# Kernel optimization log

Measured on AMD Instinct MI355X. Metric: run time of the kernel, lower is better.

## Reference

```python
import jax, jax.numpy as jnp
import numpy as np

V = 32000      # vocab_size
CTX = 1024     # context_length
D = 768        # n_embd
H = 12         # n_heads
HD = D // H    # head_dim
L = 6          # n_layers
DFF = 4 * D
B, S = 2, 1024
EPS = 1e-5


def _layernorm(x, w, b):
    mu = jnp.mean(x, axis=-1, keepdims=True)
    var = jnp.mean(jnp.square(x - mu), axis=-1, keepdims=True)
    return (x - mu) * jax.lax.rsqrt(var + EPS) * w + b


def setup_inputs() -> dict:
    key = jax.random.key(0)
    ks = iter(jax.random.split(key, 32))
    s = 0.02
    idx = jax.random.randint(next(ks), (B, S), 0, V)
    p = {
        "idx": idx,
        "tok_emb": jax.random.normal(next(ks), (V, D), jnp.float32) * s,
        "pos_emb": jax.random.normal(next(ks), (CTX, D), jnp.float32) * s,
        "ln1_w": jnp.ones((L, D)), "ln1_b": jnp.zeros((L, D)),
        "Wq": jax.random.normal(next(ks), (L, D, D), jnp.float32) * s,
        "bq": jnp.zeros((L, D)),
        "Wk": jax.random.normal(next(ks), (L, D, D), jnp.float32) * s,
        "bk": jnp.zeros((L, D)),
        "Wv": jax.random.normal(next(ks), (L, D, D), jnp.float32) * s,
        "bv": jnp.zeros((L, D)),
        "Wo": jax.random.normal(next(ks), (L, D, D), jnp.float32) * s,
        "bo": jnp.zeros((L, D)),
        "ln2_w": jnp.ones((L, D)), "ln2_b": jnp.zeros((L, D)),
        "W1": jax.random.normal(next(ks), (L, D, DFF), jnp.float32) * s,
        "b1": jnp.zeros((L, DFF)),
        "W2": jax.random.normal(next(ks), (L, DFF, D), jnp.float32) * s,
        "b2": jnp.zeros((L, D)),
        "lnf_w": jnp.ones((D,)), "lnf_b": jnp.zeros((D,)),
        "lm_head_w": jax.random.normal(next(ks), (D, V), jnp.float32) * s,
    }
    return p


def _forward(idx, tok_emb, pos_emb, ln1_w, ln1_b, Wq, bq, Wk, bk, Wv, bv,
             Wo, bo, ln2_w, ln2_b, W1, b1, W2, b2, lnf_w, lnf_b, lm_head_w):
    b, s = idx.shape
    x = tok_emb[idx] + pos_emb[:s]  # [B,S,D]
    mask = jnp.tril(jnp.ones((s, s), dtype=bool))  # causal
    scale = 1.0 / np.sqrt(HD)
    for l in range(L):
        # --- attention ---
        h = _layernorm(x, ln1_w[l], ln1_b[l])
        q = (h @ Wq[l] + bq[l]).reshape(b, s, H, HD).transpose(0, 2, 1, 3)
        k = (h @ Wk[l] + bk[l]).reshape(b, s, H, HD).transpose(0, 2, 1, 3)
        v = (h @ Wv[l] + bv[l]).reshape(b, s, H, HD).transpose(0, 2, 1, 3)
        att = jnp.einsum('bhqd,bhkd->bhqk', q, k) * scale
        att = jnp.where(mask, att, -jnp.inf)
        att = jax.nn.softmax(att, axis=-1)
        y = jnp.einsum('bhqk,bhkd->bhqd', att, v)
        y = y.transpose(0, 2, 1, 3).reshape(b, s, D)
        x = x + y @ Wo[l] + bo[l]
        # --- MLP ---
        h2 = _layernorm(x, ln2_w[l], ln2_b[l])
        x = x + jax.nn.relu(h2 @ W1[l] + b1[l]) @ W2[l] + b2[l]
    logits = _layernorm(x, lnf_w, lnf_b) @ lm_head_w  # [B,S,V]
    return logits


def reference(idx, tok_emb, pos_emb, ln1_w, ln1_b, Wq, bq, Wk, bk, Wv, bv,
              Wo, bo, ln2_w, ln2_b, W1, b1, W2, b2, lnf_w, lnf_b, lm_head_w):
    return _forward(idx, tok_emb, pos_emb, ln1_w, ln1_b, Wq, bq, Wk, bk, Wv,
                    bv, Wo, bo, ln2_w, ln2_b, W1, b1, W2, b2, lnf_w, lnf_b,
                    lm_head_w)
```

## Files before the change

### kernel.cpp

```cpp
#include <hip/hip_runtime.h>
#include <hip/hip_bf16.h>
#include <math.h>

#define D 768
#define NH 12
#define HD 64
#define NL 6
#define DFF 3072
#define BB 2
#define SS 1024
#define NROWS (BB*SS)
#define VOCAB 32000
#define QKVN (3*D)
#define LN_EPS 1e-5f

typedef __attribute__((ext_vector_type(8))) short bf16x8;
typedef __attribute__((ext_vector_type(4))) float f32x4;

typedef __attribute__((address_space(1))) const unsigned char* gas_ptr;
typedef __attribute__((address_space(3))) unsigned char* las_ptr;

__device__ __forceinline__ void load_lds16(const void* g, void* l) {
    __builtin_amdgcn_global_load_lds((gas_ptr)g, (las_ptr)l, 16, 0, 0);
}

__device__ __forceinline__ void storeOut(float* p, float v) { *p = v; }
__device__ __forceinline__ void storeOut(__hip_bfloat16* p, float v) { *p = __float2bfloat16(v); }
__device__ __forceinline__ ushort f2bs(float f) {
    __hip_bfloat16 h = __float2bfloat16(f);
    return *(ushort*)&h;
}

__global__ void embed_kernel(const int* __restrict__ idx, const float* __restrict__ tok,
                             const float* __restrict__ pos, float* __restrict__ x) {
    int row = blockIdx.x;
    int s = row % SS;
    int t = idx[row];
    for (int c = threadIdx.x; c < D; c += blockDim.x)
        x[row*D + c] = tok[(size_t)t*D + c] + pos[s*D + c];
}

template<typename OT>
__global__ __launch_bounds__(256) void layernorm_kernel(const float* __restrict__ x,
                                                        const float* __restrict__ w,
                                                        const float* __restrict__ b,
                                                        OT* __restrict__ out) {
    int row = blockIdx.x;
    __shared__ float l1[4], l2[4];
    int base = row * D;
    float vals[3];
    float s1 = 0.f, s2 = 0.f;
#pragma unroll
    for (int i = 0; i < 3; i++) {
        float v = x[base + threadIdx.x + i*256];
        vals[i] = v; s1 += v; s2 += v*v;
    }
#pragma unroll
    for (int o = 32; o > 0; o >>= 1) {
        s1 += __shfl_down(s1, o, 64);
        s2 += __shfl_down(s2, o, 64);
    }
    if ((threadIdx.x & 63) == 0) { l1[threadIdx.x >> 6] = s1; l2[threadIdx.x >> 6] = s2; }
    __syncthreads();
    float sum   = l1[0] + l1[1] + l1[2] + l1[3];
    float sumsq = l2[0] + l2[1] + l2[2] + l2[3];
    float mu  = sum * (1.f / D);
    float var = sumsq * (1.f / D) - mu * mu;
    float inv = rsqrtf(var + LN_EPS);
#pragma unroll
    for (int i = 0; i < 3; i++) {
        int c = threadIdx.x + i*256;
        storeOut(&out[base + c], (vals[i] - mu) * inv * w[c] + b[c]);
    }
}

__global__ __launch_bounds__(256) void transpose_cvt(const float* __restrict__ src,
                                                     __hip_bfloat16* __restrict__ dst,
                                                     int K, int N,
                                                     size_t srcLayerStride, size_t dstLayerStride,
                                                     int dstRowOff) {
    int l = blockIdx.z;
    src += (size_t)l * srcLayerStride;
    dst += (size_t)l * dstLayerStride + (size_t)dstRowOff * K;
    __shared__ float t[32][33];
    int k0 = blockIdx.x*32, n0 = blockIdx.y*32;
    int tx = threadIdx.x & 31, ty = threadIdx.x >> 5;
    for (int i = ty; i < 32; i += 8) t[i][tx] = src[(size_t)(k0+i)*N + n0+tx];
    __syncthreads();
    for (int i = ty; i < 32; i += 8) dst[(size_t)(n0+i)*K + k0+tx] = __float2bfloat16(t[tx][i]);
}

__global__ __launch_bounds__(256) void vtrans_kernel(const ushort* __restrict__ qkv,
                                                     ushort* __restrict__ vt) {
    int bh = blockIdx.z;
    int st = blockIdx.y;
    int dt = blockIdx.x;
    __shared__ ushort t[32][33];
    int tx = threadIdx.x & 31, ty = threadIdx.x >> 5;
    int b = bh / NH, h = bh % NH;
    int s0 = st*32, d0 = dt*32;
    for (int i = ty; i < 32; i += 8)
        t[i][tx] = qkv[(size_t)(b*SS + s0+i)*QKVN + 2*D + h*HD + d0 + tx];
    __syncthreads();
    for (int i = ty; i < 32; i += 8)
        vt[((size_t)bh*HD + d0+i)*SS + s0 + tx] = t[tx][i];
}

__global__ void pack_qkv_bias(const float* __restrict__ bq, const float* __restrict__ bk,
                              const float* __restrict__ bv, float* __restrict__ dst) {
    int l = blockIdx.y;
    int i = blockIdx.x*256 + threadIdx.x;
    dst[l*QKVN + i]         = bq[l*D + i];
    dst[l*QKVN + D + i]     = bk[l*D + i];
    dst[l*QKVN + 2*D + i]   = bv[l*D + i];
}

#define GSTAGE(buf, k0) do {                                                     \
    _Pragma("unroll")                                                            \
    for (int i_ = 0; i_ < BM/64; i_++) {                                         \
        int rt_ = wid*(BM/4) + i_*16;                                            \
        load_lds16(A + (size_t)(bm + rt_ + lrow)*K + (k0) + lcol,                \
                   &As[buf][rt_][0]);                                            \
    }                                                                            \
    _Pragma("unroll")                                                            \
    for (int i_ = 0; i_ < BN/64; i_++) {                                         \
        int rt_ = wid*(BN/4) + i_*16;                                            \
        load_lds16(BT + (size_t)(bn + rt_ + lrow)*K + (k0) + lcol,               \
                   &Bs[buf][rt_][0]);                                            \
    } } while (0)

template<int BM, int BN, int CMAJ, typename OT, int RELU, int RESID, int HASB>
__global__ __launch_bounds__(256) void gemm_mfma(const ushort* __restrict__ A,
                                                 const ushort* __restrict__ BT,
                                                 const float* __restrict__ bias,
                                                 const float* __restrict__ X,
                                                 OT* __restrict__ C,
                                                 int N, int K, int gx, int gy) {
    constexpr int WTM = BM/2, WTN = BN/2;
    constexpr int FRM = BM/32, FRN = BN/32;
    __shared__ ushort As[2][BM][32];
    __shared__ ushort Bs[2][BN][32];

    int id = blockIdx.x;
    int swz = (id & 7) * (gridDim.x >> 3) + (id >> 3);
    int bx, by;
    if (CMAJ) { bx = swz / gy; by = swz - bx * gy; }
    else      { by = swz / gx; bx = swz - by * gx; }
    int bm = by * BM, bn = bx * BN;

    int tid = threadIdx.x;
    int lane = tid & 63, wid = tid >> 6;
    int wr = wid >> 1, wc = wid & 1;
    int lrow = lane >> 2;
    int lcol = (((lane & 3) ^ (lrow & 3)) * 8);
    int fr = lane & 15, fc = lane >> 4;

    f32x4 acc[FRM][FRN];
#pragma unroll
    for (int i = 0; i < FRM; i++)
#pragma unroll
        for (int j = 0; j < FRN; j++)
#pragma unroll
            for (int r = 0; r < 4; r++) acc[i][j][r] = 0.f;

    GSTAGE(0, 0);
    asm volatile("s_waitcnt vmcnt(0)" ::: "memory");
    __syncthreads();

    int cur = 0;
    for (int t = 0; t < K/32; t++) {
        if (t*32 + 32 < K) GSTAGE(cur^1, t*32 + 32);
        bf16x8 af[FRM], bf[FRN];
#pragma unroll
        for (int mi = 0; mi < FRM; mi++)
            af[mi] = *(const bf16x8*)&As[cur][wr*WTM + mi*16 + fr][(fc ^ (fr & 3))*8];
#pragma unroll
        for (int ni = 0; ni < FRN; ni++)
            bf[ni] = *(const bf16x8*)&Bs[cur][wc*WTN + ni*16 + fr][(fc ^ (fr & 3))*8];
        __builtin_amdgcn_s_setprio(1);
#pragma unroll
        for (int mi = 0; mi < FRM; mi++)
#pragma unroll
            for (int ni = 0; ni < FRN; ni++)
                acc[mi][ni] = __builtin_amdgcn_mfma_f32_16x16x32_bf16(af[mi], bf[ni], acc[mi][ni], 0, 0, 0);
        __builtin_amdgcn_s_setprio(0);
        asm volatile("s_waitcnt vmcnt(0)" ::: "memory");
        __syncthreads();
        cur ^= 1;
    }
#pragma unroll
    for (int mi = 0; mi < FRM; mi++) {
#pragma unroll
        for (int r = 0; r < 4; r++) {
            int row = bm + wr*WTM + mi*16 + fc*4 + r;
#pragma unroll
            for (int ni = 0; ni < FRN; ni++) {
                int col = bn + wc*WTN + ni*16 + fr;
                float v = acc[mi][ni][r];
                if (HASB) v += bias[col];
                if (RESID) v += X[(size_t)row * N + col];
                if (RELU) v = fmaxf(v, 0.f);
                storeOut(&C[(size_t)row * N + col], v);
            }
        }
    }
}

#define KVSTAGE(buf, kv0) do {                                                   \
    _Pragma("unroll")                                                            \
    for (int j_ = 0; j_ < 2; j_++) {                                             \
        int r_ = w*16 + j_*8 + srow8;                                            \
        load_lds16(qkv + (size_t)(b*SS + (kv0) + r_)*QKVN + D + h*HD + schunk*8, \
                   &Ks[buf][w*16 + j_*8][0]);                                    \
        load_lds16(vt + ((size_t)(b*NH + h)*HD + r_)*SS + (kv0) + schunk*8,      \
                   &Vs[buf][w*16 + j_*8][0]);                                    \
    } } while (0)

__global__ __launch_bounds__(256) void attn_mfma(const ushort* __restrict__ qkv,
                                                 const ushort* __restrict__ vt,
                                                 __hip_bfloat16* __restrict__ y) {
    const int bx = blockIdx.x;
    const int qt = 15 - (bx & 15);
    const int h  = (bx >> 4) % NH;
    const int b  = bx / (16*NH);
    const int tid  = threadIdx.x;
    const int lane = tid & 63, w = tid >> 6;
    const int fr = lane & 15, fc = lane >> 4;

    __shared__ ushort Qs[64][64];
    __shared__ ushort Ks[2][64][64];
    __shared__ ushort Vs[2][64][64];
    __shared__ ushort Ps[4][16][72];

    const int q0 = qt * 64;
    const int srow8  = lane >> 3;
    const int schunk = (lane & 7) ^ srow8;

#pragma unroll
    for (int j = 0; j < 2; j++) {
        int r = w*16 + j*8 + srow8;
        load_lds16(qkv + (size_t)(b*SS + q0 + r)*QKVN + h*HD + schunk*8, &Qs[w*16 + j*8][0]);
    }
    KVSTAGE(0, 0);
    asm volatile("s_waitcnt vmcnt(0)" ::: "memory");
    __syncthreads();
    bf16x8 qf[2];
#pragma unroll
    for (int s = 0; s < 2; s++)
        qf[s] = *(const bf16x8*)&Qs[w*16 + fr][((s*4 + fc) ^ (fr & 7))*8];

    f32x4 oacc[4];
#pragma unroll
    for (int ni = 0; ni < 4; ni++)
#pragma unroll
        for (int r = 0; r < 4; r++) oacc[ni][r] = 0.f;
    float m[4] = {-INFINITY, -INFINITY, -INFINITY, -INFINITY};
    float l[4] = {0.f, 0.f, 0.f, 0.f};

    int cur = 0;
    for (int kt = 0; kt <= qt; kt++) {
        if (kt < qt) KVSTAGE(cur^1, (kt+1)*64);
        f32x4 sacc[4];
#pragma unroll
        for (int ni = 0; ni < 4; ni++)
#pragma unroll
            for (int r = 0; r < 4; r++) sacc[ni][r] = 0.f;
#pragma unroll
        for (int ni = 0; ni < 4; ni++)
#pragma unroll
            for (int s = 0; s < 2; s++) {
                bf16x8 kf = *(const bf16x8*)&Ks[cur][ni*16 + fr][((s*4 + fc) ^ (fr & 7))*8];
                sacc[ni] = __builtin_amdgcn_mfma_f32_16x16x32_bf16(qf[s], kf, sacc[ni], 0, 0, 0);
            }
        if (kt == qt) {
#pragma unroll
            for (int ni = 0; ni < 4; ni++)
#pragma unroll
                for (int r = 0; r < 4; r++) {
                    float v = sacc[ni][r] * 0.125f;
                    sacc[ni][r] = (ni*16 + fr > w*16 + fc*4 + r) ? -INFINITY : v;
                }
        } else {
#pragma unroll
            for (int ni = 0; ni < 4; ni++)
#pragma unroll
                for (int r = 0; r < 4; r++) sacc[ni][r] *= 0.125f;
        }
        float p[4][4];
#pragma unroll
        for (int r = 0; r < 4; r++) {
            float mx = fmaxf(fmaxf(sacc[0][r], sacc[1][r]), fmaxf(sacc[2][r], sacc[3][r]));
#pragma unroll
            for (int o = 1; o < 16; o <<= 1) mx = fmaxf(mx, __shfl_xor(mx, o, 64));
            float mn = fmaxf(m[r], mx);
            float fac = __expf(m[r] - mn);
            float rs = 0.f;
#pragma unroll
            for (int ni = 0; ni < 4; ni++) {
                float pv = __expf(sacc[ni][r] - mn);
                p[ni][r] = pv;
                rs += pv;
            }
#pragma unroll
            for (int o = 1; o < 16; o <<= 1) rs += __shfl_xor(rs, o, 64);
            l[r] = l[r] * fac + rs;
            m[r] = mn;
#pragma unroll
            for (int ni = 0; ni < 4; ni++) oacc[ni][r] *= fac;
        }
#pragma unroll
        for (int ni = 0; ni < 4; ni++)
#pragma unroll
            for (int r = 0; r < 4; r++)
                Ps[w][fc*4 + r][ni*16 + fr] = f2bs(p[ni][r]);
        bf16x8 pa[2];
#pragma unroll
        for (int s = 0; s < 2; s++) pa[s] = *(const bf16x8*)&Ps[w][fr][s*32 + fc*8];
#pragma unroll
        for (int ni = 0; ni < 4; ni++)
#pragma unroll
            for (int s = 0; s < 2; s++) {
                bf16x8 vf = *(const bf16x8*)&Vs[cur][ni*16 + fr][((s*4 + fc) ^ (fr & 7))*8];
                oacc[ni] = __builtin_amdgcn_mfma_f32_16x16x32_bf16(pa[s], vf, oacc[ni], 0, 0, 0);
            }
        asm volatile("s_waitcnt vmcnt(0)" ::: "memory");
        __syncthreads();
        cur ^= 1;
    }
#pragma unroll
    for (int r = 0; r < 4; r++) {
        float rinv = 1.f / l[r];
        int row = b*SS + q0 + w*16 + fc*4 + r;
#pragma unroll
        for (int ni = 0; ni < 4; ni++)
            y[(size_t)row*D + h*HD + ni*16 + fr] = __float2bfloat16(oacc[ni][r] * rinv);
    }
}

extern "C" void kernel_launch(void* const* d_in, const int* in_sizes, int n_in,
                              void* d_out, int out_size, void* d_ws, size_t ws_size,
                              hipStream_t stream) {
    const int*   idx  = (const int*)d_in[0];
    const float* tok  = (const float*)d_in[1];
    const float* pos  = (const float*)d_in[2];
    const float* ln1w = (const float*)d_in[3];
    const float* ln1b = (const float*)d_in[4];
    const float* Wq   = (const float*)d_in[5];
    const float* bq   = (const float*)d_in[6];
    const float* Wk   = (const float*)d_in[7];
    const float* bk   = (const float*)d_in[8];
    const float* Wv   = (const float*)d_in[9];
    const float* bv   = (const float*)d_in[10];
    const float* Wo   = (const float*)d_in[11];
    const float* bo   = (const float*)d_in[12];
    const float* ln2w = (const float*)d_in[13];
    const float* ln2b = (const float*)d_in[14];
    const float* W1   = (const float*)d_in[15];
    const float* b1   = (const float*)d_in[16];
    const float* W2   = (const float*)d_in[17];
    const float* b2   = (const float*)d_in[18];
    const float* lnfw = (const float*)d_in[19];
    const float* lnfb = (const float*)d_in[20];
    const float* lmw  = (const float*)d_in[21];
    float* out = (float*)d_out;

    char* p = (char*)d_ws;
    __hip_bfloat16* qkvT = (__hip_bfloat16*)p; p += (size_t)NL*QKVN*D*2;
    __hip_bfloat16* WoT  = (__hip_bfloat16*)p; p += (size_t)NL*D*D*2;
    __hip_bfloat16* W1T  = (__hip_bfloat16*)p; p += (size_t)NL*DFF*D*2;
    __hip_bfloat16* W2T  = (__hip_bfloat16*)p; p += (size_t)NL*D*DFF*2;
    __hip_bfloat16* lmT  = (__hip_bfloat16*)p; p += (size_t)VOCAB*D*2;
    float*          bqkv = (float*)p;          p += (size_t)NL*QKVN*4;
    float*          x    = (float*)p;          p += (size_t)NROWS*D*4;
    __hip_bfloat16* h    = (__hip_bfloat16*)p; p += (size_t)NROWS*D*2;
    __hip_bfloat16* qkv  = (__hip_bfloat16*)p; p += (size_t)NROWS*QKVN*2;
    __hip_bfloat16* vt   = (__hip_bfloat16*)p; p += (size_t)BB*NH*HD*SS*2;
    __hip_bfloat16* yb   = (__hip_bfloat16*)p; p += (size_t)NROWS*D*2;
    __hip_bfloat16* a1   = (__hip_bfloat16*)p; p += (size_t)NROWS*DFF*2;

    dim3 tDD(D/32, D/32, NL);
    transpose_cvt<<<tDD, 256, 0, stream>>>(Wq, qkvT, D, D, (size_t)D*D, (size_t)QKVN*D, 0);
    transpose_cvt<<<tDD, 256, 0, stream>>>(Wk, qkvT, D, D, (size_t)D*D, (size_t)QKVN*D, D);
    transpose_cvt<<<tDD, 256, 0, stream>>>(Wv, qkvT, D, D, (size_t)D*D, (size_t)QKVN*D, 2*D);
    transpose_cvt<<<tDD, 256, 0, stream>>>(Wo, WoT, D, D, (size_t)D*D, (size_t)D*D, 0);
    transpose_cvt<<<dim3(D/32, DFF/32, NL), 256, 0, stream>>>(W1, W1T, D, DFF, (size_t)D*DFF, (size_t)DFF*D, 0);
    transpose_cvt<<<dim3(DFF/32, D/32, NL), 256, 0, stream>>>(W2, W2T, DFF, D, (size_t)DFF*D, (size_t)D*DFF, 0);
    transpose_cvt<<<dim3(D/32, VOCAB/32, 1), 256, 0, stream>>>(lmw, lmT, D, VOCAB, 0, 0, 0);
    pack_qkv_bias<<<dim3(3, NL), 256, 0, stream>>>(bq, bk, bv, bqkv);

    embed_kernel<<<NROWS, 256, 0, stream>>>(idx, tok, pos, x);

    for (int l = 0; l < NL; l++) {
        layernorm_kernel<<<NROWS, 256, 0, stream>>>(x, ln1w + l*D, ln1b + l*D, h);
        gemm_mfma<128,64,0,__hip_bfloat16,0,0,1><<<576, 256, 0, stream>>>(
            (const ushort*)h, (const ushort*)(qkvT + (size_t)l*QKVN*D),
            bqkv + (size_t)l*QKVN, nullptr, qkv, QKVN, D, QKVN/64, NROWS/128);
        vtrans_kernel<<<dim3(2, SS/32, BB*NH), 256, 0, stream>>>((const ushort*)qkv, (ushort*)vt);
        attn_mfma<<<BB*NH*(SS/64), 256, 0, stream>>>((const ushort*)qkv, (const ushort*)vt, yb);
        gemm_mfma<64,64,0,float,0,1,1><<<384, 256, 0, stream>>>(
            (const ushort*)yb, (const ushort*)(WoT + (size_t)l*D*D),
            bo + (size_t)l*D, x, x, D, D, D/64, NROWS/64);
        layernorm_kernel<<<NROWS, 256, 0, stream>>>(x, ln2w + l*D, ln2b + l*D, h);
        gemm_mfma<128,128,0,__hip_bfloat16,1,0,1><<<384, 256, 0, stream>>>(
            (const ushort*)h, (const ushort*)(W1T + (size_t)l*DFF*D),
            b1 + (size_t)l*DFF, nullptr, a1, DFF, D, DFF/128, NROWS/128);
        gemm_mfma<64,64,0,float,0,1,1><<<384, 256, 0, stream>>>(
            (const ushort*)a1, (const ushort*)(W2T + (size_t)l*D*DFF),
            b2 + (size_t)l*D, x, x, D, DFF, D/64, NROWS/64);
    }
    layernorm_kernel<<<NROWS, 256, 0, stream>>>(x, lnfw, lnfb, h);
    gemm_mfma<128,128,1,float,0,0,0><<<4000, 256, 0, stream>>>(
        (const ushort*)h, (const ushort*)lmT, nullptr, nullptr, out, VOCAB, D,
        VOCAB/128, NROWS/128);
}
```

Before: 1.246 ms.

## Triple-buffer GEMM pipeline and fuse V transpose into QKV GEMM epilogue

The GEMM mainloop moves from double to triple buffering. It uses partial vmcnt waits and a single barrier per k-step, so global loads run further ahead of the MFMA work. The QKV GEMM epilogue now writes the V block directly in transposed layout, which removes the separate vtrans kernel and its extra read/write of V. The four Q/K/V/O weight transposes are merged into one launch. The extra LDS stage raises shared memory per block and may lower occupancy for the larger tiles.

```diff
diff --git a/kernel.cpp b/kernel.cpp
--- a/kernel.cpp
+++ b/kernel.cpp
@@ -30,6 +30,8 @@
     __hip_bfloat16 h = __float2bfloat16(f);
     return *(ushort*)&h;
 }
+
+#define WAIT_VMCNT(n) asm volatile("s_waitcnt vmcnt(" #n ")" ::: "memory")
 
 __global__ void embed_kernel(const int* __restrict__ idx, const float* __restrict__ tok,
                              const float* __restrict__ pos, float* __restrict__ x) {
@@ -90,20 +92,22 @@
     for (int i = ty; i < 32; i += 8) dst[(size_t)(n0+i)*K + k0+tx] = __float2bfloat16(t[tx][i]);
 }
 
-__global__ __launch_bounds__(256) void vtrans_kernel(const ushort* __restrict__ qkv,
-                                                     ushort* __restrict__ vt) {
-    int bh = blockIdx.z;
-    int st = blockIdx.y;
-    int dt = blockIdx.x;
-    __shared__ ushort t[32][33];
+__global__ __launch_bounds__(256) void qkvo_trans(const float* __restrict__ Wq,
+                                                  const float* __restrict__ Wk,
+                                                  const float* __restrict__ Wv,
+                                                  const float* __restrict__ Wo,
+                                                  __hip_bfloat16* __restrict__ qkvT,
+                                                  __hip_bfloat16* __restrict__ WoT) {
+    int z = blockIdx.z, l = z >> 2, m = z & 3;
+    const float* src = (m==0 ? Wq : m==1 ? Wk : m==2 ? Wv : Wo) + (size_t)l*D*D;
+    __hip_bfloat16* dst = (m < 3) ? qkvT + (size_t)l*QKVN*D + (size_t)m*D*D
+                                  : WoT  + (size_t)l*D*D;
+    __shared__ float t[32][33];
+    int k0 = blockIdx.x*32, n0 = blockIdx.y*32;
     int tx = threadIdx.x & 31, ty = threadIdx.x >> 5;
-    int b = bh / NH, h = bh % NH;
-    int s0 = st*32, d0 = dt*32;
-    for (int i = ty; i < 32; i += 8)
-        t[i][tx] = qkv[(size_t)(b*SS + s0+i)*QKVN + 2*D + h*HD + d0 + tx];
+    for (int i = ty; i < 32; i += 8) t[i][tx] = src[(size_t)(k0+i)*D + n0+tx];
     __syncthreads();
-    for (int i = ty; i < 32; i += 8)
-        vt[((size_t)bh*HD + d0+i)*SS + s0 + tx] = t[tx][i];
+    for (int i = ty; i < 32; i += 8) dst[(size_t)(n0+i)*D + k0+tx] = __float2bfloat16(t[tx][i]);
 }
 
 __global__ void pack_qkv_bias(const float* __restrict__ bq, const float* __restrict__ bk,
@@ -129,17 +133,19 @@
                    &Bs[buf][rt_][0]);                                            \
     } } while (0)
 
-template<int BM, int BN, int CMAJ, typename OT, int RELU, int RESID, int HASB>
+template<int BM, int BN, int CMAJ, typename OT, int RELU, int RESID, int HASB, int VSTORE>
 __global__ __launch_bounds__(256) void gemm_mfma(const ushort* __restrict__ A,
                                                  const ushort* __restrict__ BT,
                                                  const float* __restrict__ bias,
                                                  const float* __restrict__ X,
                                                  OT* __restrict__ C,
+                                                 ushort* __restrict__ vt,
                                                  int N, int K, int gx, int gy) {
     constexpr int WTM = BM/2, WTN = BN/2;
     constexpr int FRM = BM/32, FRN = BN/32;
-    __shared__ ushort As[2][BM][32];
-    __shared__ ushort Bs[2][BN][32];
+    constexpr int LPS = BM/64 + BN/64;
+    __shared__ ushort As[3][BM][32];
+    __shared__ ushort Bs[3][BN][32];
 
     int id = blockIdx.x;
     int swz = (id & 7) * (gridDim.x >> 3) + (id >> 3);
@@ -163,13 +169,25 @@
 #pragma unroll
             for (int r = 0; r < 4; r++) acc[i][j][r] = 0.f;
 
+    const int NT = K / 32;
     GSTAGE(0, 0);
-    asm volatile("s_waitcnt vmcnt(0)" ::: "memory");
-    __syncthreads();
+    GSTAGE(1, 32);
 
     int cur = 0;
-    for (int t = 0; t < K/32; t++) {
-        if (t*32 + 32 < K) GSTAGE(cur^1, t*32 + 32);
+    for (int t = 0; t < NT; t++) {
+        if (t + 1 < NT) {
+            if constexpr (LPS == 2) WAIT_VMCNT(2);
+            else if constexpr (LPS == 3) WAIT_VMCNT(3);
+            else WAIT_VMCNT(4);
+        } else {
+            WAIT_VMCNT(0);
+        }
+        __builtin_amdgcn_s_barrier();
+        asm volatile("" ::: "memory");
+        if (t + 2 < NT) {
+            int nb = cur >= 1 ? cur - 1 : cur + 2;
+            GSTAGE(nb, (t+2)*32);
+        }
         bf16x8 af[FRM], bf[FRN];
 #pragma unroll
         for (int mi = 0; mi < FRM; mi++)
@@ -184,23 +202,44 @@
             for (int ni = 0; ni < FRN; ni++)
                 acc[mi][ni] = __builtin_amdgcn_mfma_f32_16x16x32_bf16(af[mi], bf[ni], acc[mi][ni], 0, 0, 0);
         __builtin_amdgcn_s_setprio(0);
-        asm volatile("s_waitcnt vmcnt(0)" ::: "memory");
-        __syncthreads();
-        cur ^= 1;
-    }
-#pragma unroll
-    for (int mi = 0; mi < FRM; mi++) {
-#pragma unroll
-        for (int r = 0; r < 4; r++) {
-            int row = bm + wr*WTM + mi*16 + fc*4 + r;
+        cur = cur < 2 ? cur + 1 : 0;
+    }
+
+    if (VSTORE && bn >= 2*D) {
+        int hh = (bn - 2*D) / HD;
+        int b  = bm >> 10;
+        size_t vbase = ((size_t)(b*NH + hh)) * HD;
+        int srow0 = (bm & (SS-1)) + wr*WTM + fc*4;
+#pragma unroll
+        for (int mi = 0; mi < FRM; mi++) {
 #pragma unroll
             for (int ni = 0; ni < FRN; ni++) {
                 int col = bn + wc*WTN + ni*16 + fr;
-                float v = acc[mi][ni][r];
-                if (HASB) v += bias[col];
-                if (RESID) v += X[(size_t)row * N + col];
-                if (RELU) v = fmaxf(v, 0.f);
-                storeOut(&C[(size_t)row * N + col], v);
+                int d   = wc*WTN + ni*16 + fr;
+                float bv_ = bias[col];
+                ushort4 u;
+                u.x = f2bs(acc[mi][ni][0] + bv_);
+                u.y = f2bs(acc[mi][ni][1] + bv_);
+                u.z = f2bs(acc[mi][ni][2] + bv_);
+                u.w = f2bs(acc[mi][ni][3] + bv_);
+                *(ushort4*)&vt[(vbase + d)*SS + srow0 + mi*16] = u;
+            }
+        }
+    } else {
+#pragma unroll
+        for (int mi = 0; mi < FRM; mi++) {
+#pragma unroll
+            for (int r = 0; r < 4; r++) {
+                int row = bm + wr*WTM + mi*16 + fc*4 + r;
+#pragma unroll
+                for (int ni = 0; ni < FRN; ni++) {
+                    int col = bn + wc*WTN + ni*16 + fr;
+                    float v = acc[mi][ni][r];
+                    if (HASB) v += bias[col];
+                    if (RESID) v += X[(size_t)row * N + col];
+                    if (RELU) v = fmaxf(v, 0.f);
+                    storeOut(&C[(size_t)row * N + col], v);
+                }
             }
         }
     }
@@ -378,11 +417,7 @@
     __hip_bfloat16* yb   = (__hip_bfloat16*)p; p += (size_t)NROWS*D*2;
     __hip_bfloat16* a1   = (__hip_bfloat16*)p; p += (size_t)NROWS*DFF*2;
 
-    dim3 tDD(D/32, D/32, NL);
-    transpose_cvt<<<tDD, 256, 0, stream>>>(Wq, qkvT, D, D, (size_t)D*D, (size_t)QKVN*D, 0);
-    transpose_cvt<<<tDD, 256, 0, stream>>>(Wk, qkvT, D, D, (size_t)D*D, (size_t)QKVN*D, D);
-    transpose_cvt<<<tDD, 256, 0, stream>>>(Wv, qkvT, D, D, (size_t)D*D, (size_t)QKVN*D, 2*D);
-    transpose_cvt<<<tDD, 256, 0, stream>>>(Wo, WoT, D, D, (size_t)D*D, (size_t)D*D, 0);
+    qkvo_trans<<<dim3(D/32, D/32, NL*4), 256, 0, stream>>>(Wq, Wk, Wv, Wo, qkvT, WoT);
     transpose_cvt<<<dim3(D/32, DFF/32, NL), 256, 0, stream>>>(W1, W1T, D, DFF, (size_t)D*DFF, (size_t)DFF*D, 0);
     transpose_cvt<<<dim3(DFF/32, D/32, NL), 256, 0, stream>>>(W2, W2T, DFF, D, (size_t)DFF*D, (size_t)D*DFF, 0);
     transpose_cvt<<<dim3(D/32, VOCAB/32, 1), 256, 0, stream>>>(lmw, lmT, D, VOCAB, 0, 0, 0);
@@ -392,24 +427,23 @@
 
     for (int l = 0; l < NL; l++) {
         layernorm_kernel<<<NROWS, 256, 0, stream>>>(x, ln1w + l*D, ln1b + l*D, h);
-        gemm_mfma<128,64,0,__hip_bfloat16,0,0,1><<<576, 256, 0, stream>>>(
+        gemm_mfma<128,64,0,__hip_bfloat16,0,0,1,1><<<576, 256, 0, stream>>>(
             (const ushort*)h, (const ushort*)(qkvT + (size_t)l*QKVN*D),
-            bqkv + (size_t)l*QKVN, nullptr, qkv, QKVN, D, QKVN/64, NROWS/128);
-        vtrans_kernel<<<dim3(2, SS/32, BB*NH), 256, 0, stream>>>((const ushort*)qkv, (ushort*)vt);
+            bqkv + (size_t)l*QKVN, nullptr, qkv, (ushort*)vt, QKVN, D, QKVN/64, NROWS/128);
         attn_mfma<<<BB*NH*(SS/64), 256, 0, stream>>>((const ushort*)qkv, (const ushort*)vt, yb);
-        gemm_mfma<64,64,0,float,0,1,1><<<384, 256, 0, stream>>>(
+        gemm_mfma<64,64,0,float,0,1,1,0><<<384, 256, 0, stream>>>(
             (const ushort*)yb, (const ushort*)(WoT + (size_t)l*D*D),
-            bo + (size_t)l*D, x, x, D, D, D/64, NROWS/64);
+            bo + (size_t)l*D, x, x, nullptr, D, D, D/64, NROWS/64);
         layernorm_kernel<<<NROWS, 256, 0, stream>>>(x, ln2w + l*D, ln2b + l*D, h);
-        gemm_mfma<128,128,0,__hip_bfloat16,1,0,1><<<384, 256, 0, stream>>>(
+        gemm_mfma<128,128,0,__hip_bfloat16,1,0,1,0><<<384, 256, 0, stream>>>(
             (const ushort*)h, (const ushort*)(W1T + (size_t)l*DFF*D),
-            b1 + (size_t)l*DFF, nullptr, a1, DFF, D, DFF/128, NROWS/128);
-        gemm_mfma<64,64,0,float,0,1,1><<<384, 256, 0, stream>>>(
+            b1 + (size_t)l*DFF, nullptr, a1, nullptr, DFF, D, DFF/128, NROWS/128);
+        gemm_mfma<64,64,0,float,0,1,1,0><<<384, 256, 0, stream>>>(
             (const ushort*)a1, (const ushort*)(W2T + (size_t)l*D*DFF),
-            b2 + (size_t)l*D, x, x, D, DFF, D/64, NROWS/64);
+            b2 + (size_t)l*D, x, x, nullptr, D, DFF, D/64, NROWS/64);
     }
     layernorm_kernel<<<NROWS, 256, 0, stream>>>(x, lnfw, lnfb, h);
-    gemm_mfma<128,128,1,float,0,0,0><<<4000, 256, 0, stream>>>(
-        (const ushort*)h, (const ushort*)lmT, nullptr, nullptr, out, VOCAB, D,
+    gemm_mfma<128,128,1,float,0,0,0,0><<<4000, 256, 0, stream>>>(
+        (const ushort*)h, (const ushort*)lmT, nullptr, nullptr, out, nullptr, VOCAB, D,
         VOCAB/128, NROWS/128);
 }
```

After: 1.251 ms. No clear change (+0.4%).
